# Performance work log

Hardware: AMD Instinct MI355X
Metric: run time of the kernel (lower is better)

## Reference

```python
import jax, jax.numpy as jnp
import numpy as np

N_NODES = 50000
N_EDGES = 600000
IN_FEATS = 16
H_FEAT = 128
N_CLASSES = 4
N_HIDDEN_LAYERS = 19  # conv2..conv20


def setup_inputs() -> dict:
    key = jax.random.key(0)
    ks = jax.random.split(key, 10)
    x = jax.random.normal(ks[0], (N_NODES, IN_FEATS), dtype=jnp.float32)
    edge_index = jax.random.randint(ks[1], (2, N_EDGES), 0, N_NODES, dtype=jnp.int32)
    edge_attr = jax.random.uniform(ks[2], (N_EDGES, 1), dtype=jnp.float32)
    s_in = 1.0 / np.sqrt(IN_FEATS)
    s_h = 1.0 / np.sqrt(H_FEAT)
    W_in = jax.random.uniform(ks[3], (IN_FEATS, H_FEAT), minval=-s_in, maxval=s_in, dtype=jnp.float32)
    b_in = jax.random.uniform(ks[4], (H_FEAT,), minval=-s_in, maxval=s_in, dtype=jnp.float32)
    W_h = jax.random.uniform(ks[5], (N_HIDDEN_LAYERS, H_FEAT, H_FEAT), minval=-s_h, maxval=s_h, dtype=jnp.float32)
    b_h = jax.random.uniform(ks[6], (N_HIDDEN_LAYERS, H_FEAT), minval=-s_h, maxval=s_h, dtype=jnp.float32)
    W_fc = jax.random.uniform(ks[7], (H_FEAT, N_CLASSES), minval=-s_h, maxval=s_h, dtype=jnp.float32)
    b_fc = jax.random.uniform(ks[8], (N_CLASSES,), minval=-s_h, maxval=s_h, dtype=jnp.float32)
    return {"x": x, "edge_index": edge_index, "edge_attr": edge_attr,
            "W_in": W_in, "b_in": b_in, "W_h": W_h, "b_h": b_h,
            "W_fc": W_fc, "b_fc": b_fc}


def reference(x, edge_index, edge_attr, W_in, b_in, W_h, b_h, W_fc, b_fc):
    src, dst = edge_index[0], edge_index[1]
    ew = edge_attr[:, 0]  # edge_weight = edge_attr[:, 0]
    n = x.shape[0]
    # degree by dst, clamped at 1
    deg = jax.ops.segment_sum(jnp.ones(src.shape[0], dtype=x.dtype), dst, num_segments=n)
    deg_inv = 1.0 / jnp.maximum(deg, 1.0)  # [N]

    def conv(h, W, b):
        h = h @ W + b                       # [N, out]
        msg = h[src] * ew[:, None]          # [E, out]
        agg = jax.ops.segment_sum(msg, dst, num_segments=n)
        return agg * deg_inv[:, None]

    h = jax.nn.leaky_relu(conv(x, W_in, b_in))

    def step(h, params):
        W, b = params
        return jax.nn.leaky_relu(conv(h, W, b)), None

    h, _ = jax.lax.scan(step, h, (W_h, b_h))
    return h @ W_fc + b_fc  # [N, num_classes]
```

## Files before the change

kernel.cpp:

```cpp
#include <hip/hip_runtime.h>
#include <hip/hip_fp16.h>

#define N_NODES 50000
#define N_EDGES 600000
#define IN_F 16
#define HF 128
#define NC 4
#define NHL 19
#define N_FP8_LAYERS 17
#define WS_STRIDE 136

__device__ __forceinline__ float lrelu(float x) { return x > 0.f ? x : 0.01f * x; }

struct h4 { __half2 a, b; };

typedef _Float16 f16;
typedef _Float16 f16x8 __attribute__((ext_vector_type(8)));
typedef float    f32x4 __attribute__((ext_vector_type(4)));
typedef float    f32x2 __attribute__((ext_vector_type(2)));

__device__ __forceinline__ unsigned pack_fp8x4(float a, float b, float c, float d) {
    int r = __builtin_amdgcn_cvt_pk_fp8_f32(a, b, 0, false);
    r = __builtin_amdgcn_cvt_pk_fp8_f32(c, d, r, true);
    return (unsigned)r;
}


__global__ void count_deg_k(const int* __restrict__ dst, int* __restrict__ cnt) {
    int e = blockIdx.x * 256 + threadIdx.x;
    if (e < N_EDGES) atomicAdd(&cnt[dst[e]], 1);
}

__global__ void scan_k(const int* __restrict__ cnt, int* __restrict__ rowptr,
                       float* __restrict__ dinv) {
    __shared__ int wsum[16];
    __shared__ int carry_s;
    int t = threadIdx.x;
    int lane = t & 63, wid = t >> 6;
    if (t == 0) carry_s = 0;
    __syncthreads();
    for (int base = 0; base < N_NODES; base += 4096) {
        int idx = base + t * 4;
        int4 v = make_int4(0, 0, 0, 0);
        if (idx + 3 < N_NODES) v = *(const int4*)&cnt[idx];
        else {
            if (idx     < N_NODES) v.x = cnt[idx];
            if (idx + 1 < N_NODES) v.y = cnt[idx + 1];
            if (idx + 2 < N_NODES) v.z = cnt[idx + 2];
            if (idx + 3 < N_NODES) v.w = cnt[idx + 3];
        }
        if (idx + 3 < N_NODES) {
            float4 dv = make_float4(1.f / fmaxf((float)v.x, 1.f), 1.f / fmaxf((float)v.y, 1.f),
                                    1.f / fmaxf((float)v.z, 1.f), 1.f / fmaxf((float)v.w, 1.f));
            *(float4*)&dinv[idx] = dv;
        } else {
            if (idx     < N_NODES) dinv[idx]     = 1.f / fmaxf((float)v.x, 1.f);
            if (idx + 1 < N_NODES) dinv[idx + 1] = 1.f / fmaxf((float)v.y, 1.f);
            if (idx + 2 < N_NODES) dinv[idx + 2] = 1.f / fmaxf((float)v.z, 1.f);
            if (idx + 3 < N_NODES) dinv[idx + 3] = 1.f / fmaxf((float)v.w, 1.f);
        }
        int s1 = v.x + v.y, s2 = s1 + v.z, total = s2 + v.w;
        int sc = total;
#pragma unroll
        for (int off = 1; off < 64; off <<= 1) {
            int u = __shfl_up(sc, off, 64);
            if (lane >= off) sc += u;
        }
        if (lane == 63) wsum[wid] = sc;
        __syncthreads();
        if (t < 16) {
            int w = wsum[t];
#pragma unroll
            for (int off = 1; off < 16; off <<= 1) {
                int u = __shfl_up(w, off, 64);
                if (t >= off) w += u;
            }
            wsum[t] = w;
        }
        __syncthreads();
        int prefix = carry_s + (wid > 0 ? wsum[wid - 1] : 0) + (sc - total);
        if (idx     < N_NODES) rowptr[idx]     = prefix;
        if (idx + 1 < N_NODES) rowptr[idx + 1] = prefix + v.x;
        if (idx + 2 < N_NODES) rowptr[idx + 2] = prefix + s1;
        if (idx + 3 < N_NODES) rowptr[idx + 3] = prefix + s2;
        __syncthreads();
        if (t == 0) carry_s += wsum[15];
        __syncthreads();
    }
    if (t == 0) rowptr[N_NODES] = carry_s;
}

__global__ void fill_k(const int* __restrict__ src, const int* __restrict__ dst,
                       const float* __restrict__ ea, const int* __restrict__ rowptr,
                       int* __restrict__ fill, int2* __restrict__ edg,
                       const float* __restrict__ dinv) {
    int e = blockIdx.x * 256 + threadIdx.x;
    if (e < N_EDGES) {
        int d = dst[e];
        int pos = rowptr[d] + atomicAdd(&fill[d], 1);
        edg[pos] = make_int2(src[e], __float_as_int(ea[e] * dinv[d]));
    }
}


__global__ void wconv_k(const float* __restrict__ Wh, __half* __restrict__ Wt) {
    int idx = blockIdx.x * 256 + threadIdx.x;
    if (idx >= NHL * HF * HF) return;
    int l = idx / (HF * HF);
    int r = idx - l * (HF * HF);
    int n = r >> 7;
    int k = r & 127;
    Wt[idx] = __float2half(Wh[(size_t)l * HF * HF + k * HF + n]);
}


__global__ void gemm_in_k(const float* __restrict__ X, const float* __restrict__ W,
                          const float* __restrict__ b, unsigned* __restrict__ T8) {
    __shared__ float Ws[IN_F * HF];
    int t = threadIdx.x;
    ((float4*)Ws)[t]       = ((const float4*)W)[t];
    ((float4*)Ws)[t + 256] = ((const float4*)W)[t + 256];
    __syncthreads();
    int row = blockIdx.x * 16 + (t >> 4);
    if (row >= N_NODES) return;
    int tx = t & 15;
    int c0 = tx * 4, c1 = 64 + tx * 4;
    float4 a0 = *(const float4*)&b[c0];
    float4 a1 = *(const float4*)&b[c1];
    const float4* xr = (const float4*)(X + row * IN_F);
#pragma unroll
    for (int k4 = 0; k4 < 4; k4++) {
        float4 xv = xr[k4];
        const float* xp = (const float*)&xv;
#pragma unroll
        for (int kk = 0; kk < 4; kk++) {
            int k = k4 * 4 + kk;
            float4 w0 = *(const float4*)&Ws[k * HF + c0];
            float4 w1 = *(const float4*)&Ws[k * HF + c1];
            float xs = xp[kk];
            a0.x = fmaf(xs, w0.x, a0.x); a0.y = fmaf(xs, w0.y, a0.y);
            a0.z = fmaf(xs, w0.z, a0.z); a0.w = fmaf(xs, w0.w, a0.w);
            a1.x = fmaf(xs, w1.x, a1.x); a1.y = fmaf(xs, w1.y, a1.y);
            a1.z = fmaf(xs, w1.z, a1.z); a1.w = fmaf(xs, w1.w, a1.w);
        }
    }
    T8[(size_t)row * 32 + tx]      = pack_fp8x4(a0.x, a0.y, a0.z, a0.w);
    T8[(size_t)row * 32 + 16 + tx] = pack_fp8x4(a1.x, a1.y, a1.z, a1.w);
}


template <bool FP8IN, bool FP8OUT>
__global__ __launch_bounds__(256) void gemm_mfma_k(const void* __restrict__ Hin,
                                                   const __half* __restrict__ Wt,
                                                   const float* __restrict__ b,
                                                   void* __restrict__ Tout) {
    __shared__ __half Ws[HF * WS_STRIDE];
    __shared__ __half Hs[64 * WS_STRIDE];
    int t = threadIdx.x;
    int rbase = blockIdx.x * 64;
    int u16 = t & 15;
    int rg  = t >> 4;

#pragma unroll
    for (int p = 0; p < 8; p++) {
        int n = p * 16 + rg;
        *(float4*)&Ws[n * WS_STRIDE + u16 * 8] = *(const float4*)&Wt[(size_t)n * HF + u16 * 8];
    }
#pragma unroll
    for (int p = 0; p < 4; p++) {
        int rl = p * 16 + rg;
        int row = rbase + rl;
        if (row >= N_NODES) row = N_NODES - 1;
        if (FP8IN) {
            uint2 hv8 = *(const uint2*)&((const unsigned char*)Hin)[(size_t)row * HF + u16 * 8];
            f32x2 a0 = __builtin_amdgcn_cvt_pk_f32_fp8((int)hv8.x, false);
            f32x2 a1 = __builtin_amdgcn_cvt_pk_f32_fp8((int)hv8.x, true);
            f32x2 a2 = __builtin_amdgcn_cvt_pk_f32_fp8((int)hv8.y, false);
            f32x2 a3 = __builtin_amdgcn_cvt_pk_f32_fp8((int)hv8.y, true);
            h4 o0, o1;
            o0.a = __floats2half2_rn(a0.x, a0.y); o0.b = __floats2half2_rn(a1.x, a1.y);
            o1.a = __floats2half2_rn(a2.x, a2.y); o1.b = __floats2half2_rn(a3.x, a3.y);
            float4 pk;
            ((h4*)&pk)[0] = o0;
            *(h4*)((char*)&pk + 8) = o1;
            *(float4*)&Hs[rl * WS_STRIDE + u16 * 8] = pk;
        } else {
            *(float4*)&Hs[rl * WS_STRIDE + u16 * 8] =
                *(const float4*)&((const __half*)Hin)[(size_t)row * HF + u16 * 8];
        }
    }
    __syncthreads();

    int lane = t & 63;
    int w    = t >> 6;
    int wr   = w * 16;
    int m16  = lane & 15;
    int q    = lane >> 4;

    f16x8 af[4];
#pragma unroll
    for (int kc = 0; kc < 4; kc++)
        af[kc] = *(const f16x8*)&Hs[(wr + m16) * WS_STRIDE + kc * 32 + q * 8];

    f32x4 acc[8];
#pragma unroll
    for (int nt = 0; nt < 8; nt++) {
        float bv = b[nt * 16 + m16];
        acc[nt] = (f32x4){bv, bv, bv, bv};
#pragma unroll
        for (int kc = 0; kc < 4; kc++) {
            f16x8 bf = *(const f16x8*)&Ws[(nt * 16 + m16) * WS_STRIDE + kc * 32 + q * 8];
            acc[nt] = __builtin_amdgcn_mfma_f32_16x16x32_f16(af[kc], bf, acc[nt], 0, 0, 0);
        }
    }
    __syncthreads();

#pragma unroll
    for (int nt = 0; nt < 8; nt++)
#pragma unroll
        for (int r = 0; r < 4; r++)
            Hs[(wr + q * 4 + r) * WS_STRIDE + nt * 16 + m16] = __float2half(acc[nt][r]);
    __syncthreads();

#pragma unroll
    for (int p = 0; p < 4; p++) {
        int rl = p * 16 + rg;
        int row = rbase + rl;
        if (row < N_NODES) {
            float4 cv = *(float4*)&Hs[rl * WS_STRIDE + u16 * 8];
            if (FP8OUT) {
                __half2* hp = (__half2*)&cv;
                float2 f0 = __half22float2(hp[0]);
                float2 f1 = __half22float2(hp[1]);
                float2 f2 = __half22float2(hp[2]);
                float2 f3 = __half22float2(hp[3]);
                uint2 o;
                o.x = pack_fp8x4(f0.x, f0.y, f1.x, f1.y);
                o.y = pack_fp8x4(f2.x, f2.y, f3.x, f3.y);
                *(uint2*)&((unsigned char*)Tout)[(size_t)row * HF + u16 * 8] = o;
            } else {
                *(float4*)&((__half*)Tout)[(size_t)row * HF + u16 * 8] = cv;
            }
        }
    }
}


template <bool FP8IN, bool FP8OUT>
__global__ __launch_bounds__(256) void agg4_k(const void* __restrict__ Tin,
                                              void* __restrict__ O,
                                              const int* __restrict__ rowptr,
                                              const int2* __restrict__ edg) {
    int gw = blockIdx.x * 4 + (threadIdx.x >> 6);
    int v0 = gw * 4;
    if (v0 >= N_NODES) return;
    int lane = threadIdx.x & 63;
    int q  = lane >> 4;
    int li = lane & 15;

    int rp = rowptr[v0 + min(lane, 4)];
    int r0 = __shfl(rp, 0, 64), r1 = __shfl(rp, 1, 64), r2 = __shfl(rp, 2, 64);
    int r3 = __shfl(rp, 3, 64), r4 = __shfl(rp, 4, 64);
    int e0 = __shfl(rp, q, 64);
    int e1 = __shfl(rp, q + 1, 64);
    int degmax = max(max(r1 - r0, r2 - r1), max(r3 - r2, r4 - r3));
    int nb = (degmax + 15) >> 4;

    const uint2* T8  = (const uint2*)Tin;
    const uint4* T16 = (const uint4*)Tin;

    float acc[8] = {0.f, 0.f, 0.f, 0.f, 0.f, 0.f, 0.f, 0.f};

    for (int eb = 0; eb < nb; eb++) {
        int idx = e0 + eb * 16 + li;
        bool ok = idx < e1;
        int2 rec = edg[ok ? idx : 0];
        if (!ok) rec.y = 0;
        int sb = q << 4;
#pragma unroll
        for (int g = 0; g < 2; g++) {
            int   ss[8];
            float ww[8];
#pragma unroll
            for (int u = 0; u < 8; u++) {
                int sl = sb + g * 8 + u;
                ss[u] = __shfl(rec.x, sl, 64);
                ww[u] = __int_as_float(__shfl(rec.y, sl, 64));
            }
            if (FP8IN) {
                uint2 gv[8];
#pragma unroll
                for (int u = 0; u < 8; u++)
                    gv[u] = T8[(size_t)ss[u] * 16 + li];
#pragma unroll
                for (int u = 0; u < 8; u++) {
                    f32x2 p0 = __builtin_amdgcn_cvt_pk_f32_fp8((int)gv[u].x, false);
                    f32x2 p1 = __builtin_amdgcn_cvt_pk_f32_fp8((int)gv[u].x, true);
                    f32x2 p2 = __builtin_amdgcn_cvt_pk_f32_fp8((int)gv[u].y, false);
                    f32x2 p3 = __builtin_amdgcn_cvt_pk_f32_fp8((int)gv[u].y, true);
                    acc[0] = fmaf(p0.x, ww[u], acc[0]);
                    acc[1] = fmaf(p0.y, ww[u], acc[1]);
                    acc[2] = fmaf(p1.x, ww[u], acc[2]);
                    acc[3] = fmaf(p1.y, ww[u], acc[3]);
                    acc[4] = fmaf(p2.x, ww[u], acc[4]);
                    acc[5] = fmaf(p2.y, ww[u], acc[5]);
                    acc[6] = fmaf(p3.x, ww[u], acc[6]);
                    acc[7] = fmaf(p3.y, ww[u], acc[7]);
                }
            } else {
                uint4 gv[8];
#pragma unroll
                for (int u = 0; u < 8; u++)
                    gv[u] = T16[(size_t)ss[u] * 16 + li];
#pragma unroll
                for (int u = 0; u < 8; u++) {
                    __half2* hp = (__half2*)&gv[u];
                    float2 p0 = __half22float2(hp[0]);
                    float2 p1 = __half22float2(hp[1]);
                    float2 p2 = __half22float2(hp[2]);
                    float2 p3 = __half22float2(hp[3]);
                    acc[0] = fmaf(p0.x, ww[u], acc[0]);
                    acc[1] = fmaf(p0.y, ww[u], acc[1]);
                    acc[2] = fmaf(p1.x, ww[u], acc[2]);
                    acc[3] = fmaf(p1.y, ww[u], acc[3]);
                    acc[4] = fmaf(p2.x, ww[u], acc[4]);
                    acc[5] = fmaf(p2.y, ww[u], acc[5]);
                    acc[6] = fmaf(p3.x, ww[u], acc[6]);
                    acc[7] = fmaf(p3.y, ww[u], acc[7]);
                }
            }
        }
    }
    int v = v0 + q;
    if (FP8OUT) {
        uint2 o;
        o.x = pack_fp8x4(lrelu(acc[0]), lrelu(acc[1]), lrelu(acc[2]), lrelu(acc[3]));
        o.y = pack_fp8x4(lrelu(acc[4]), lrelu(acc[5]), lrelu(acc[6]), lrelu(acc[7]));
        ((uint2*)O)[(size_t)v * 16 + li] = o;
    } else {
        h4 oa, ob;
        oa.a = __floats2half2_rn(lrelu(acc[0]), lrelu(acc[1]));
        oa.b = __floats2half2_rn(lrelu(acc[2]), lrelu(acc[3]));
        ob.a = __floats2half2_rn(lrelu(acc[4]), lrelu(acc[5]));
        ob.b = __floats2half2_rn(lrelu(acc[6]), lrelu(acc[7]));
        uint4 ov;
        ((h4*)&ov)[0] = oa;
        *(h4*)((char*)&ov + 8) = ob;
        ((uint4*)O)[(size_t)v * 16 + li] = ov;
    }
}


__global__ void fc_k(const __half* __restrict__ H, const float* __restrict__ W,
                     const float* __restrict__ b, float* __restrict__ out) {
    int r = blockIdx.x * 256 + threadIdx.x;
    if (r >= N_NODES) return;
    float4 acc = *(const float4*)b;
    const h4* hp = (const h4*)(H + (size_t)r * HF);
    const float4* w4 = (const float4*)W;
#pragma unroll
    for (int k4 = 0; k4 < 32; k4++) {
        h4 hh = hp[k4];
        float2 p0 = __half22float2(hh.a);
        float2 p1 = __half22float2(hh.b);
        float4 wa = w4[k4 * 4 + 0], wb = w4[k4 * 4 + 1];
        float4 wc = w4[k4 * 4 + 2], wd = w4[k4 * 4 + 3];
        acc.x = fmaf(p0.x, wa.x, acc.x); acc.y = fmaf(p0.x, wa.y, acc.y);
        acc.z = fmaf(p0.x, wa.z, acc.z); acc.w = fmaf(p0.x, wa.w, acc.w);
        acc.x = fmaf(p0.y, wb.x, acc.x); acc.y = fmaf(p0.y, wb.y, acc.y);
        acc.z = fmaf(p0.y, wb.z, acc.z); acc.w = fmaf(p0.y, wb.w, acc.w);
        acc.x = fmaf(p1.x, wc.x, acc.x); acc.y = fmaf(p1.x, wc.y, acc.y);
        acc.z = fmaf(p1.x, wc.z, acc.z); acc.w = fmaf(p1.x, wc.w, acc.w);
        acc.x = fmaf(p1.y, wd.x, acc.x); acc.y = fmaf(p1.y, wd.y, acc.y);
        acc.z = fmaf(p1.y, wd.z, acc.z); acc.w = fmaf(p1.y, wd.w, acc.w);
    }
    *(float4*)&out[r * NC] = acc;
}


extern "C" void kernel_launch(void* const* d_in, const int* in_sizes, int n_in,
                              void* d_out, int out_size, void* d_ws, size_t ws_size,
                              hipStream_t stream) {
    const float* X   = (const float*)d_in[0];
    const int*   EI  = (const int*)d_in[1];
    const float* EA  = (const float*)d_in[2];
    const float* Win = (const float*)d_in[3];
    const float* bin = (const float*)d_in[4];
    const float* Wh  = (const float*)d_in[5];
    const float* bh  = (const float*)d_in[6];
    const float* Wfc = (const float*)d_in[7];
    const float* bfc = (const float*)d_in[8];
    float* out = (float*)d_out;
    const int* src = EI;
    const int* dst = EI + N_EDGES;

    char* ws = (char*)d_ws;
    size_t off = 0;
    void*   O   = (void*)(ws + off);   off += (size_t)N_NODES * HF * 2;
    void*   T   = (void*)(ws + off);   off += (size_t)N_NODES * HF * 2;
    __half* Wt  = (__half*)(ws + off); off += (size_t)NHL * HF * HF * 2;
    int2* edg   = (int2*)(ws + off);  off += (size_t)N_EDGES * 8;
    int* rowptr = (int*)(ws + off);   off += (((size_t)(N_NODES + 1) * 4 + 15) / 16) * 16;
    int* cnt    = (int*)(ws + off);   off += (size_t)N_NODES * 4;
    int* fill   = (int*)(ws + off);   off += (size_t)N_NODES * 4;
    float* dinv = (float*)(ws + off); off += (size_t)N_NODES * 4;

    hipMemsetAsync(cnt, 0, N_NODES * 4, stream);
    hipMemsetAsync(fill, 0, N_NODES * 4, stream);
    count_deg_k<<<(N_EDGES + 255) / 256, 256, 0, stream>>>(dst, cnt);
    scan_k<<<1, 1024, 0, stream>>>(cnt, rowptr, dinv);
    fill_k<<<(N_EDGES + 255) / 256, 256, 0, stream>>>(src, dst, EA, rowptr, fill, edg, dinv);
    wconv_k<<<(NHL * HF * HF + 255) / 256, 256, 0, stream>>>(Wh, Wt);

    const int aggg  = (N_NODES / 4 + 3) / 4;
    const int gemmg = (N_NODES + 63) / 64;

    gemm_in_k<<<(N_NODES + 15) / 16, 256, 0, stream>>>(X, Win, bin, (unsigned*)T);
    agg4_k<true, true><<<aggg, 256, 0, stream>>>(T, O, rowptr, edg);
    for (int l = 0; l < N_FP8_LAYERS; l++) {
        gemm_mfma_k<true, true><<<gemmg, 256, 0, stream>>>(
            O, Wt + (size_t)l * HF * HF, bh + (size_t)l * HF, T);
        if (l < N_FP8_LAYERS - 1)
            agg4_k<true, true><<<aggg, 256, 0, stream>>>(T, O, rowptr, edg);
        else
            agg4_k<true, false><<<aggg, 256, 0, stream>>>(T, O, rowptr, edg);
    }
    for (int l = N_FP8_LAYERS; l < NHL; l++) {
        gemm_mfma_k<false, false><<<gemmg, 256, 0, stream>>>(
            O, Wt + (size_t)l * HF * HF, bh + (size_t)l * HF, T);
        agg4_k<false, false><<<aggg, 256, 0, stream>>>(T, O, rowptr, edg);
    }
    fc_k<<<(N_NODES + 255) / 256, 256, 0, stream>>>((const __half*)O, Wfc, bfc, out);
}
```

Baseline: 705.7 us.

## Split FP8 feature matrix into two column halves for cache-friendlier gathers

Stores the FP8 node-feature tensors as two planar halves of 64 columns each instead of interleaved 128-byte rows. The FP8 aggregation kernel is replaced by a half-width version launched with twice the blocks, each block gathering only one half. Each pass then works on a 3.2 MB working set that is more likely to stay in L2/MALL during random neighbour gathers. The cost is twice the edge-list and rowptr reads and 4-byte instead of 8-byte gather loads per lane.

```diff
diff --git a/kernel.cpp b/kernel.cpp
--- a/kernel.cpp
+++ b/kernel.cpp
@@ -9,6 +9,7 @@
 #define NHL 19
 #define N_FP8_LAYERS 17
 #define WS_STRIDE 136
+#define GRIDH ((N_NODES + 15) / 16)
 
 __device__ __forceinline__ float lrelu(float x) { return x > 0.f ? x : 0.01f * x; }
 
@@ -24,6 +25,8 @@
     r = __builtin_amdgcn_cvt_pk_fp8_f32(c, d, r, true);
     return (unsigned)r;
 }
+
+#define FP8_HALF_STRIDE ((size_t)N_NODES * 16)
 
 
 __global__ void count_deg_k(const int* __restrict__ dst, int* __restrict__ cnt) {
@@ -144,8 +147,8 @@
             a1.z = fmaf(xs, w1.z, a1.z); a1.w = fmaf(xs, w1.w, a1.w);
         }
     }
-    T8[(size_t)row * 32 + tx]      = pack_fp8x4(a0.x, a0.y, a0.z, a0.w);
-    T8[(size_t)row * 32 + 16 + tx] = pack_fp8x4(a1.x, a1.y, a1.z, a1.w);
+    T8[(size_t)row * 16 + tx]                   = pack_fp8x4(a0.x, a0.y, a0.z, a0.w);
+    T8[FP8_HALF_STRIDE + (size_t)row * 16 + tx] = pack_fp8x4(a1.x, a1.y, a1.z, a1.w);
 }
 
 
@@ -172,7 +175,10 @@
         int row = rbase + rl;
         if (row >= N_NODES) row = N_NODES - 1;
         if (FP8IN) {
-            uint2 hv8 = *(const uint2*)&((const unsigned char*)Hin)[(size_t)row * HF + u16 * 8];
+            int hh  = u16 >> 3;
+            int o16 = u16 & 7;
+            const unsigned* Hb = (const unsigned*)Hin + (size_t)hh * FP8_HALF_STRIDE;
+            uint2 hv8 = *(const uint2*)&Hb[(size_t)row * 16 + o16 * 2];
             f32x2 a0 = __builtin_amdgcn_cvt_pk_f32_fp8((int)hv8.x, false);
             f32x2 a1 = __builtin_amdgcn_cvt_pk_f32_fp8((int)hv8.x, true);
             f32x2 a2 = __builtin_amdgcn_cvt_pk_f32_fp8((int)hv8.y, false);
@@ -237,7 +243,10 @@
                 uint2 o;
                 o.x = pack_fp8x4(f0.x, f0.y, f1.x, f1.y);
                 o.y = pack_fp8x4(f2.x, f2.y, f3.x, f3.y);
-                *(uint2*)&((unsigned char*)Tout)[(size_t)row * HF + u16 * 8] = o;
+                int hh  = u16 >> 3;
+                int o16 = u16 & 7;
+                unsigned* Tb = (unsigned*)Tout + (size_t)hh * FP8_HALF_STRIDE;
+                *(uint2*)&Tb[(size_t)row * 16 + o16 * 2] = o;
             } else {
                 *(float4*)&((__half*)Tout)[(size_t)row * HF + u16 * 8] = cv;
             }
@@ -246,7 +255,77 @@
 }
 
 
-template <bool FP8IN, bool FP8OUT>
+template <bool FP8OUT>
+__global__ __launch_bounds__(256) void agg4h_k(const unsigned* __restrict__ T8,
+                                               void* __restrict__ O,
+                                               const int* __restrict__ rowptr,
+                                               const int2* __restrict__ edg) {
+    int b = blockIdx.x;
+    int half = (b >= GRIDH) ? 1 : 0;
+    int gw = (b - half * GRIDH) * 4 + (threadIdx.x >> 6);
+    int v0 = gw * 4;
+    if (v0 >= N_NODES) return;
+    int lane = threadIdx.x & 63;
+    int q  = lane >> 4;
+    int li = lane & 15;
+
+    int rp = rowptr[v0 + min(lane, 4)];
+    int r0 = __shfl(rp, 0, 64), r1 = __shfl(rp, 1, 64), r2 = __shfl(rp, 2, 64);
+    int r3 = __shfl(rp, 3, 64), r4 = __shfl(rp, 4, 64);
+    int e0 = __shfl(rp, q, 64);
+    int e1 = __shfl(rp, q + 1, 64);
+    int degmax = max(max(r1 - r0, r2 - r1), max(r3 - r2, r4 - r3));
+    int nb = (degmax + 15) >> 4;
+
+    const unsigned* Tb = T8 + (size_t)half * FP8_HALF_STRIDE;
+
+    float acc[4] = {0.f, 0.f, 0.f, 0.f};
+
+    for (int eb = 0; eb < nb; eb++) {
+        int idx = e0 + eb * 16 + li;
+        bool ok = idx < e1;
+        int2 rec = edg[ok ? idx : 0];
+        if (!ok) rec.y = 0;
+        int sb = q << 4;
+#pragma unroll
+        for (int g = 0; g < 2; g++) {
+            int   ss[8];
+            float ww[8];
+#pragma unroll
+            for (int u = 0; u < 8; u++) {
+                int sl = sb + g * 8 + u;
+                ss[u] = __shfl(rec.x, sl, 64);
+                ww[u] = __int_as_float(__shfl(rec.y, sl, 64));
+            }
+            unsigned gv[8];
+#pragma unroll
+            for (int u = 0; u < 8; u++)
+                gv[u] = Tb[(size_t)ss[u] * 16 + li];
+#pragma unroll
+            for (int u = 0; u < 8; u++) {
+                f32x2 lo = __builtin_amdgcn_cvt_pk_f32_fp8((int)gv[u], false);
+                f32x2 hi = __builtin_amdgcn_cvt_pk_f32_fp8((int)gv[u], true);
+                acc[0] = fmaf(lo.x, ww[u], acc[0]);
+                acc[1] = fmaf(lo.y, ww[u], acc[1]);
+                acc[2] = fmaf(hi.x, ww[u], acc[2]);
+                acc[3] = fmaf(hi.y, ww[u], acc[3]);
+            }
+        }
+    }
+    int v = v0 + q;
+    if (FP8OUT) {
+        unsigned* Ob = (unsigned*)O + (size_t)half * FP8_HALF_STRIDE;
+        Ob[(size_t)v * 16 + li] =
+            pack_fp8x4(lrelu(acc[0]), lrelu(acc[1]), lrelu(acc[2]), lrelu(acc[3]));
+    } else {
+        h4 o;
+        o.a = __floats2half2_rn(lrelu(acc[0]), lrelu(acc[1]));
+        o.b = __floats2half2_rn(lrelu(acc[2]), lrelu(acc[3]));
+        ((h4*)O)[(size_t)v * 32 + half * 16 + li] = o;
+    }
+}
+
+
 __global__ __launch_bounds__(256) void agg4_k(const void* __restrict__ Tin,
                                               void* __restrict__ O,
                                               const int* __restrict__ rowptr,
@@ -266,7 +345,6 @@
     int degmax = max(max(r1 - r0, r2 - r1), max(r3 - r2, r4 - r3));
     int nb = (degmax + 15) >> 4;
 
-    const uint2* T8  = (const uint2*)Tin;
     const uint4* T16 = (const uint4*)Tin;
 
     float acc[8] = {0.f, 0.f, 0.f, 0.f, 0.f, 0.f, 0.f, 0.f};
@@ -287,67 +365,38 @@
                 ss[u] = __shfl(rec.x, sl, 64);
                 ww[u] = __int_as_float(__shfl(rec.y, sl, 64));
             }
-            if (FP8IN) {
-                uint2 gv[8];
-#pragma unroll
-                for (int u = 0; u < 8; u++)
-                    gv[u] = T8[(size_t)ss[u] * 16 + li];
-#pragma unroll
-                for (int u = 0; u < 8; u++) {
-                    f32x2 p0 = __builtin_amdgcn_cvt_pk_f32_fp8((int)gv[u].x, false);
-                    f32x2 p1 = __builtin_amdgcn_cvt_pk_f32_fp8((int)gv[u].x, true);
-                    f32x2 p2 = __builtin_amdgcn_cvt_pk_f32_fp8((int)gv[u].y, false);
-                    f32x2 p3 = __builtin_amdgcn_cvt_pk_f32_fp8((int)gv[u].y, true);
-                    acc[0] = fmaf(p0.x, ww[u], acc[0]);
-                    acc[1] = fmaf(p0.y, ww[u], acc[1]);
-                    acc[2] = fmaf(p1.x, ww[u], acc[2]);
-                    acc[3] = fmaf(p1.y, ww[u], acc[3]);
-                    acc[4] = fmaf(p2.x, ww[u], acc[4]);
-                    acc[5] = fmaf(p2.y, ww[u], acc[5]);
-                    acc[6] = fmaf(p3.x, ww[u], acc[6]);
-                    acc[7] = fmaf(p3.y, ww[u], acc[7]);
-                }
-            } else {
-                uint4 gv[8];
-#pragma unroll
-                for (int u = 0; u < 8; u++)
-                    gv[u] = T16[(size_t)ss[u] * 16 + li];
-#pragma unroll
-                for (int u = 0; u < 8; u++) {
-                    __half2* hp = (__half2*)&gv[u];
-                    float2 p0 = __half22float2(hp[0]);
-                    float2 p1 = __half22float2(hp[1]);
-                    float2 p2 = __half22float2(hp[2]);
-                    float2 p3 = __half22float2(hp[3]);
-                    acc[0] = fmaf(p0.x, ww[u], acc[0]);
-                    acc[1] = fmaf(p0.y, ww[u], acc[1]);
-                    acc[2] = fmaf(p1.x, ww[u], acc[2]);
-                    acc[3] = fmaf(p1.y, ww[u], acc[3]);
-                    acc[4] = fmaf(p2.x, ww[u], acc[4]);
-                    acc[5] = fmaf(p2.y, ww[u], acc[5]);
-                    acc[6] = fmaf(p3.x, ww[u], acc[6]);
-                    acc[7] = fmaf(p3.y, ww[u], acc[7]);
-                }
+            uint4 gv[8];
+#pragma unroll
+            for (int u = 0; u < 8; u++)
+                gv[u] = T16[(size_t)ss[u] * 16 + li];
+#pragma unroll
+            for (int u = 0; u < 8; u++) {
+                __half2* hp = (__half2*)&gv[u];
+                float2 p0 = __half22float2(hp[0]);
+                float2 p1 = __half22float2(hp[1]);
+                float2 p2 = __half22float2(hp[2]);
+                float2 p3 = __half22float2(hp[3]);
+                acc[0] = fmaf(p0.x, ww[u], acc[0]);
+                acc[1] = fmaf(p0.y, ww[u], acc[1]);
+                acc[2] = fmaf(p1.x, ww[u], acc[2]);
+                acc[3] = fmaf(p1.y, ww[u], acc[3]);
+                acc[4] = fmaf(p2.x, ww[u], acc[4]);
+                acc[5] = fmaf(p2.y, ww[u], acc[5]);
+                acc[6] = fmaf(p3.x, ww[u], acc[6]);
+                acc[7] = fmaf(p3.y, ww[u], acc[7]);
             }
         }
     }
     int v = v0 + q;
-    if (FP8OUT) {
-        uint2 o;
-        o.x = pack_fp8x4(lrelu(acc[0]), lrelu(acc[1]), lrelu(acc[2]), lrelu(acc[3]));
-        o.y = pack_fp8x4(lrelu(acc[4]), lrelu(acc[5]), lrelu(acc[6]), lrelu(acc[7]));
-        ((uint2*)O)[(size_t)v * 16 + li] = o;
-    } else {
-        h4 oa, ob;
-        oa.a = __floats2half2_rn(lrelu(acc[0]), lrelu(acc[1]));
-        oa.b = __floats2half2_rn(lrelu(acc[2]), lrelu(acc[3]));
-        ob.a = __floats2half2_rn(lrelu(acc[4]), lrelu(acc[5]));
-        ob.b = __floats2half2_rn(lrelu(acc[6]), lrelu(acc[7]));
-        uint4 ov;
-        ((h4*)&ov)[0] = oa;
-        *(h4*)((char*)&ov + 8) = ob;
-        ((uint4*)O)[(size_t)v * 16 + li] = ov;
-    }
+    h4 oa, ob;
+    oa.a = __floats2half2_rn(lrelu(acc[0]), lrelu(acc[1]));
+    oa.b = __floats2half2_rn(lrelu(acc[2]), lrelu(acc[3]));
+    ob.a = __floats2half2_rn(lrelu(acc[4]), lrelu(acc[5]));
+    ob.b = __floats2half2_rn(lrelu(acc[6]), lrelu(acc[7]));
+    uint4 ov;
+    ((h4*)&ov)[0] = oa;
+    *(h4*)((char*)&ov + 8) = ob;
+    ((uint4*)O)[(size_t)v * 16 + li] = ov;
 }
 
 
@@ -412,23 +461,24 @@
     fill_k<<<(N_EDGES + 255) / 256, 256, 0, stream>>>(src, dst, EA, rowptr, fill, edg, dinv);
     wconv_k<<<(NHL * HF * HF + 255) / 256, 256, 0, stream>>>(Wh, Wt);
 
+    const int agghg = 2 * GRIDH;
     const int aggg  = (N_NODES / 4 + 3) / 4;
     const int gemmg = (N_NODES + 63) / 64;
 
     gemm_in_k<<<(N_NODES + 15) / 16, 256, 0, stream>>>(X, Win, bin, (unsigned*)T);
-    agg4_k<true, true><<<aggg, 256, 0, stream>>>(T, O, rowptr, edg);
+    agg4h_k<true><<<agghg, 256, 0, stream>>>((const unsigned*)T, O, rowptr, edg);
     for (int l = 0; l < N_FP8_LAYERS; l++) {
         gemm_mfma_k<true, true><<<gemmg, 256, 0, stream>>>(
             O, Wt + (size_t)l * HF * HF, bh + (size_t)l * HF, T);
         if (l < N_FP8_LAYERS - 1)
-            agg4_k<true, true><<<aggg, 256, 0, stream>>>(T, O, rowptr, edg);
+            agg4h_k<true><<<agghg, 256, 0, stream>>>((const unsigned*)T, O, rowptr, edg);
         else
-            agg4_k<true, false><<<aggg, 256, 0, stream>>>(T, O, rowptr, edg);
+            agg4h_k<false><<<agghg, 256, 0, stream>>>((const unsigned*)T, O, rowptr, edg);
     }
     for (int l = N_FP8_LAYERS; l < NHL; l++) {
         gemm_mfma_k<false, false><<<gemmg, 256, 0, stream>>>(
             O, Wt + (size_t)l * HF * HF, bh + (size_t)l * HF, T);
-        agg4_k<false, false><<<aggg, 256, 0, stream>>>(T, O, rowptr, edg);
+        agg4_k<<<aggg, 256, 0, stream>>>(T, O, rowptr, edg);
     }
     fc_k<<<(N_NODES + 255) / 256, 256, 0, stream>>>((const __half*)O, Wfc, bfc, out);
 }
```

Measured after the change: 738.6 us. +4.7%, slower.
